# Optimization experiments

Hardware: AMD Instinct MI355X
Metric: run time of the kernel (lower is better)

## Reference

```python
import jax, jax.numpy as jnp
import numpy as np

B, N, L, D = 64, 512, 12, 128   # batch, nodes, neighbors, node_dim==edge_dim
Z = 3 * D                        # 2*node_dim + edge_dim
NC = 3                           # n_convs
VOCAB = 1000
BN_EPS = 1e-3                    # keras BatchNormalization default epsilon


def setup_inputs() -> dict:
    key = jax.random.key(0)
    ks = jax.random.split(key, 14)
    inp = {}
    inp['node_types'] = jax.random.randint(ks[0], (B, N), 0, VOCAB)
    inp['neighbor_list'] = jax.random.randint(ks[1], (B, N, L), 0, N)
    inp['edge_types'] = jax.random.randint(ks[2], (B, N, L), 0, VOCAB)
    inp['slot_types'] = jax.random.normal(ks[3], (B, N, D), jnp.float32)
    inp['node_w'] = jax.random.normal(ks[4], (VOCAB, D), jnp.float32) * 0.1
    inp['edge_w'] = jax.random.normal(ks[5], (VOCAB, D), jnp.float32) * 0.1
    inp['wf'] = jax.random.normal(ks[6], (NC, Z, D), jnp.float32) * 0.05
    inp['bf'] = jax.random.normal(ks[7], (NC, D), jnp.float32) * 0.01
    inp['ws'] = jax.random.normal(ks[8], (NC, Z, D), jnp.float32) * 0.05
    inp['bs'] = jax.random.normal(ks[9], (NC, D), jnp.float32) * 0.01
    inp['bn_gamma'] = jnp.ones((NC, D), jnp.float32)
    inp['bn_beta'] = jnp.zeros((NC, D), jnp.float32)
    inp['bn_mean'] = jax.random.normal(ks[10], (NC, D), jnp.float32) * 0.01
    inp['bn_var'] = jax.random.uniform(ks[11], (NC, D), jnp.float32, 0.5, 1.5)
    inp['dense_w'] = jax.random.normal(ks[12], (D, 1), jnp.float32) * 0.1
    inp['dense_b'] = jnp.zeros((1,), jnp.float32)
    return inp


def _embed(w, x):
    # gather with negative-index masking, as in Embedding.call (inference path)
    idx = jnp.where(x < 0, 0, x)
    mask = (x >= 0).astype(jnp.float32)[..., None]
    return w[idx] * mask


def reference(node_types, neighbor_list, edge_types, slot_types,
              node_w, edge_w, wf, bf, ws, bs,
              bn_gamma, bn_beta, bn_mean, bn_var, dense_w, dense_b):
    v = _embed(node_w, node_types) + slot_types          # (B, N, D)
    e = _embed(edge_w, edge_types)                       # (B, N, L, D)

    nl = neighbor_list
    n_safe = jnp.where(nl < 0, 0, nl)                    # (B, N, L)
    nmask = (nl >= 0).astype(jnp.float32)[..., None]     # (B, N, L, 1)

    for i in range(NC):
        # neighbor gather: per-batch index into node axis
        nn = jax.vmap(lambda vv, ii: vv[ii])(v, n_safe) * nmask  # (B, N, L, D)
        v_view = jnp.broadcast_to(v[:, :, None, :], nn.shape)
        z = jnp.concatenate([v_view, nn, e], axis=-1)            # (B, N, L, Z)
        s = (jax.nn.sigmoid(jnp.einsum('bnlz,zd->bnld', z, wf[i]) + bf[i])
             * jnp.tanh(jnp.einsum('bnlz,zd->bnld', z, ws[i]) + bs[i])
             * nmask)
        v_next = v + jnp.sum(s, axis=2)                          # (B, N, D)

        # masked batchnorm (inference: moving stats); invalid rows -> 0
        vf = v_next.reshape(-1, D)
        valid = jnp.all(jnp.abs(vf) > 1e-5, axis=-1)
        bn = bn_gamma[i] * (vf - bn_mean[i]) * jax.lax.rsqrt(bn_var[i] + BN_EPS) + bn_beta[i]
        v = jnp.where(valid[:, None], bn, 0.0).reshape(B, N, D)

    # masked mean pooling over nodes
    pmask = (node_types >= 0).astype(jnp.float32)[..., None]     # (B, N, 1)
    pooled = jnp.sum(v * pmask, axis=1) / jnp.sum(pmask, axis=1)  # (B, D)
    return pooled @ dense_w + dense_b                            # (B, 1)
```

## Files before the change

### kernel.cpp

```cpp
#include <hip/hip_runtime.h>

#define NB 64
#define NN 512
#define NL 12
#define ND 128
#define NZ 384
#define NCONV 3
#define VOCAB 1000
#define BN_EPS 1e-3f
#define LO_SCALE 2048.0f
#define INV_LO (1.0f/2048.0f)
#define SCF (-1.4426950408889634f)
#define SCS ( 2.8853900817779268f)

typedef _Float16 f16;
using half8 = __attribute__((ext_vector_type(8))) _Float16;
using floatx16 = __attribute__((ext_vector_type(16))) float;

__device__ __forceinline__ floatx16 mfma32(half8 a, half8 b, floatx16 c) {
    return __builtin_amdgcn_mfma_f32_32x32x16_f16(a, b, c, 0, 0, 0);
}
__device__ __forceinline__ void split1(float x, f16& h, f16& l) {
    h = (f16)x; l = (f16)((x - (float)h) * LO_SCALE);
}

__global__ __launch_bounds__(256) void setup_kernel(
    const float* __restrict__ wf, const float* __restrict__ wsg,
    f16* __restrict__ Wc_hi, f16* __restrict__ Wc_lo,
    const float* __restrict__ edge_w, float* __restrict__ EWp,
    const int* __restrict__ node_types, const float* __restrict__ slot_types,
    const float* __restrict__ node_w, f16* __restrict__ vhi, f16* __restrict__ vlo)
{
    __shared__ float se[32][128];
    const int blk = blockIdx.x;
    const int tid = threadIdx.x;
    if (blk < 768) {
        int id = blk * 256 + tid;
        int c = id >> 16;
        int rem = id & 65535;
        int col = rem >> 7, k = rem & 127;
        int part = col >> 7;
        int d = col & 127;
        int z = (part < 2) ? (128 + k) : k;
        const float* W = (part & 1) ? wsg : wf;
        float wv = W[((size_t)c * NZ + z) * ND + d];
        f16 h, l; split1(wv, h, l);
        size_t dst = (size_t)c * 65536 + (size_t)(k >> 3) * 4096 + col * 8 + (k & 7);
        Wc_hi[dst] = h; Wc_lo[dst] = l;
    } else if (blk < 864) {
        const int bid = blk - 768;
        const int c = bid >> 5;
        const int tyg = (bid & 31) * 32;
        for (int i = tid; i < 4096; i += 256) {
            int ty = i >> 7, k = i & 127;
            int tyv = tyg + ty;
            se[ty][k] = (tyv < VOCAB) ? edge_w[(size_t)tyv * ND + k] : 0.f;
        }
        __syncthreads();
        const int h = tid >> 7, col = tid & 127;
        const float* W = h ? wsg : wf;
        const float sc = h ? SCS : SCF;
        float acc[32];
        #pragma unroll
        for (int ty = 0; ty < 32; ++ty) acc[ty] = 0.f;
        #pragma unroll 4
        for (int k = 0; k < 128; ++k) {
            float wv = W[((size_t)c * NZ + 256 + k) * ND + col];
            #pragma unroll
            for (int ty = 0; ty < 32; ++ty) acc[ty] = fmaf(se[ty][k], wv, acc[ty]);
        }
        #pragma unroll
        for (int ty = 0; ty < 32; ++ty) {
            int tyv = tyg + ty;
            if (tyv <= VOCAB)
                EWp[((size_t)c * (VOCAB + 1) + tyv) * 256 + (col & 63) * 4 + (col >> 6) * 2 + h] = acc[ty] * sc;
        }
    } else {
        int i = (blk - 864) * 256 + tid;
        int bn = i >> 7, d = i & 127;
        int ty = node_types[bn];
        float m = ty >= 0 ? 1.f : 0.f;
        int idx = ty >= 0 ? ty : 0;
        float v = node_w[(size_t)idx * ND + d] * m + slot_types[i];
        f16 h, l; split1(v, h, l);
        vhi[i] = h; vlo[i] = l;
    }
}

__global__ __launch_bounds__(256, 3) void psgemm_kernel(
    const f16* __restrict__ vhi, const f16* __restrict__ vlo,
    const f16* __restrict__ Wc_hi, const f16* __restrict__ Wc_lo,
    const float* __restrict__ bfv, const float* __restrict__ bsv,
    float* __restrict__ Ppk, float* __restrict__ Spk)
{
    __shared__ __align__(16) char sA[16384];
    const int hw = blockIdx.x;
    const int xcd = hw & 7;
    const int q = hw >> 3;
    const int bl = q >> 5;
    const int r = q & 31;
    const int half = r >> 4;
    const int xloc = r & 15;
    const int batch = bl * 8 + xcd;
    const int node0 = batch * NN + xloc * 32;

    const int tid = threadIdx.x;
    const int lane = tid & 63, w = tid >> 6;
    const int l31 = lane & 31, l32 = lane >> 5;

    #pragma unroll
    for (int it = 0; it < 2; ++it) {
        int slot = it * 256 + tid;
        int rr = slot >> 4, cc = slot & 15;
        int cs = cc ^ (rr & 15);
        size_t src = (size_t)(node0 + rr) * ND + cs * 8;
        *(half8*)(sA + rr * 256 + cc * 16) = *(const half8*)(vhi + src);
        *(half8*)(sA + 8192 + rr * 256 + cc * 16) = *(const half8*)(vlo + src);
    }
    __syncthreads();

    const int dcol = w * 32 + l31;
    const int col0 = half * 256 + dcol;
    const int col1 = col0 + 128;

    floatx16 a00 = {}, a10 = {}, a01 = {}, a11 = {};

    int ch0 = l32;
    half8 b0h = *(const half8*)(Wc_hi + (size_t)ch0 * 4096 + col0 * 8);
    half8 b0l = *(const half8*)(Wc_lo + (size_t)ch0 * 4096 + col0 * 8);
    half8 b1h = *(const half8*)(Wc_hi + (size_t)ch0 * 4096 + col1 * 8);
    half8 b1l = *(const half8*)(Wc_lo + (size_t)ch0 * 4096 + col1 * 8);

    #pragma unroll
    for (int ks = 0; ks < 8; ++ks) {
        half8 n0h, n0l, n1h, n1l;
        if (ks < 7) {
            int nch = (ks + 1) * 2 + l32;
            n0h = *(const half8*)(Wc_hi + (size_t)nch * 4096 + col0 * 8);
            n0l = *(const half8*)(Wc_lo + (size_t)nch * 4096 + col0 * 8);
            n1h = *(const half8*)(Wc_hi + (size_t)nch * 4096 + col1 * 8);
            n1l = *(const half8*)(Wc_lo + (size_t)nch * 4096 + col1 * 8);
        }
        int qq = (((ks * 2 + l32) ^ (l31 & 15)) << 4);
        half8 ah = *(const half8*)(sA + l31 * 256 + qq);
        half8 al = *(const half8*)(sA + 8192 + l31 * 256 + qq);
        a00 = mfma32(ah, b0h, a00);
        a10 = mfma32(ah, b0l, a10);
        a10 = mfma32(al, b0h, a10);
        a01 = mfma32(ah, b1h, a01);
        a11 = mfma32(ah, b1l, a11);
        a11 = mfma32(al, b1h, a11);
        b0h = n0h; b0l = n0l; b1h = n1h; b1l = n1l;
    }

    float bx = 0.f, by = 0.f;
    if (half) { bx = bfv[dcol]; by = bsv[dcol]; }
    float* outp = half ? Spk : Ppk;
    const int dsub = (dcol & 63) * 4 + (dcol >> 6) * 2;
    #pragma unroll
    for (int rr = 0; rr < 16; ++rr) {
        int orow = (rr & 3) + 8 * (rr >> 2) + 4 * l32;
        float2 v2 = { (a00[rr] + a10[rr] * INV_LO + bx) * SCF,
                      (a01[rr] + a11[rr] * INV_LO + by) * SCS };
        *(float2*)(outp + (size_t)(node0 + orow) * 256 + dsub) = v2;
    }
}

__global__ __launch_bounds__(256, 4) void edge_epilogue_kernel(
    f16* __restrict__ vhi, f16* __restrict__ vlo,
    const int* __restrict__ neighbor_list, const int* __restrict__ edge_types,
    const float* __restrict__ Ppk, const float* __restrict__ Spk,
    const float* __restrict__ EWp,
    const float* __restrict__ bn_gamma, const float* __restrict__ bn_beta,
    const float* __restrict__ bn_mean, const float* __restrict__ bn_var)
{
    __shared__ float s_red[2][64][2];
    const int hw = blockIdx.x;
    const int xcd = hw & 7;
    const int q = hw >> 3;
    const int b = (q >> 8) * 8 + xcd;
    const int j = q & 255;
    const int node0 = b * NN + j * 2;

    const int tid = threadIdx.x;
    const int w = tid >> 6, ds = tid & 63;
    const int nl_ = w >> 1;
    const int sub = w & 1;
    const int node = node0 + nl_;
    const int bbase = b * NN;

    int nlv = -1, etv = -1;
    if (ds < 6) {
        nlv = neighbor_list[node * NL + sub * 6 + ds];
        etv = edge_types[node * NL + sub * 6 + ds];
    }
    unsigned long long bm = __ballot(nlv >= 0);

    float4 sp4 = *(const float4*)(Spk + (size_t)node * 256 + ds * 4);
    float4 p4[6], e4[6];
    #pragma unroll
    for (int l = 0; l < 6; ++l) {
        int nl_l = __builtin_amdgcn_readlane(nlv, l);
        int et_l = __builtin_amdgcn_readlane(etv, l);
        int ns = (nl_l >= 0) ? (bbase + nl_l) : node;
        int es = (et_l >= 0) ? et_l : VOCAB;
        p4[l] = *(const float4*)(Ppk + (size_t)ns * 256 + ds * 4);
        e4[l] = *(const float4*)(EWp + (size_t)es * 256 + ds * 4);
    }

    float sum0 = 0.f, sum1 = 0.f;
    #pragma unroll
    for (int l = 0; l < 6; ++l) {
        float m = ((bm >> l) & 1) ? 1.f : 0.f;
        float ax = p4[l].x + sp4.x + e4[l].x;
        float ay = p4[l].y + sp4.y + e4[l].y;
        float az = p4[l].z + sp4.z + e4[l].z;
        float aw = p4[l].w + sp4.w + e4[l].w;
        float u0 = __builtin_amdgcn_exp2f(fminf(ax, 60.f));
        float w0 = __builtin_amdgcn_exp2f(fminf(ay, 60.f));
        float u1 = __builtin_amdgcn_exp2f(fminf(az, 60.f));
        float w1 = __builtin_amdgcn_exp2f(fminf(aw, 60.f));
        float r0 = __builtin_amdgcn_rcpf(fmaf(u0, w0, 1.f + u0 + w0));
        float r1 = __builtin_amdgcn_rcpf(fmaf(u1, w1, 1.f + u1 + w1));
        sum0 = fmaf((w0 - 1.f) * r0, m, sum0);
        sum1 = fmaf((w1 - 1.f) * r1, m, sum1);
    }

    if (sub) { s_red[nl_][ds][0] = sum0; s_red[nl_][ds][1] = sum1; }
    __syncthreads();
    if (!sub) {
        sum0 += s_red[nl_][ds][0];
        sum1 += s_red[nl_][ds][1];
        size_t i0 = (size_t)node * ND + ds;
        size_t i1 = i0 + 64;
        float x0 = (float)vhi[i0] + (float)vlo[i0] * INV_LO + sum0;
        float x1 = (float)vhi[i1] + (float)vlo[i1] * INV_LO + sum1;
        int valid = __all(fabsf(x0) > 1e-5f && fabsf(x1) > 1e-5f);

        float gm0 = bn_gamma[ds], be0 = bn_beta[ds], mu0 = bn_mean[ds];
        float gm1 = bn_gamma[ds + 64], be1 = bn_beta[ds + 64], mu1 = bn_mean[ds + 64];
        float rs0 = __builtin_amdgcn_rcpf(sqrtf(bn_var[ds] + BN_EPS));
        float rs1 = __builtin_amdgcn_rcpf(sqrtf(bn_var[ds + 64] + BN_EPS));
        float o0 = valid ? (gm0 * (x0 - mu0) * rs0 + be0) : 0.f;
        float o1 = valid ? (gm1 * (x1 - mu1) * rs1 + be1) : 0.f;
        f16 h, l2;
        split1(o0, h, l2); vhi[i0] = h; vlo[i0] = l2;
        split1(o1, h, l2); vhi[i1] = h; vlo[i1] = l2;
    }
}

__global__ __launch_bounds__(256) void pool1_kernel(
    const f16* __restrict__ vhi, const f16* __restrict__ vlo,
    const int* __restrict__ node_types, float* __restrict__ partial)
{
    __shared__ float sbuf[128];
    const int b = blockIdx.x >> 3, chunk = blockIdx.x & 7;
    const int d = threadIdx.x & 127, sub = threadIdx.x >> 7;
    const int n0 = chunk * 64 + sub * 32;
    float sum = 0.f;
    #pragma unroll 4
    for (int i = 0; i < 32; ++i) {
        int n = n0 + i;
        int ty = node_types[b * NN + n];
        float mk = ty >= 0 ? 1.f : 0.f;
        size_t ix = ((size_t)(b * NN + n)) * ND + d;
        sum += ((float)vhi[ix] + (float)vlo[ix] * INV_LO) * mk;
    }
    if (sub == 0) sbuf[d] = sum;
    __syncthreads();
    if (sub == 1) partial[(size_t)blockIdx.x * 128 + d] = sbuf[d] + sum;
}

__global__ __launch_bounds__(128) void pool2_kernel(
    const float* __restrict__ partial, const int* __restrict__ node_types,
    const float* __restrict__ dense_w, const float* __restrict__ dense_b,
    float* __restrict__ out)
{
    __shared__ float s_part[2], s_cnt[2];
    const int b = blockIdx.x;
    const int d = threadIdx.x;
    float sum = 0.f;
    #pragma unroll
    for (int c = 0; c < 8; ++c) sum += partial[(size_t)(b * 8 + c) * 128 + d];
    float cnt = 0.f;
    #pragma unroll
    for (int i = 0; i < 4; ++i)
        cnt += (node_types[b * NN + d + i * 128] >= 0) ? 1.f : 0.f;
    #pragma unroll
    for (int off = 32; off > 0; off >>= 1) cnt += __shfl_xor(cnt, off);
    if ((d & 63) == 0) s_cnt[d >> 6] = cnt;
    __syncthreads();
    float tcnt = s_cnt[0] + s_cnt[1];
    float pv = (sum / tcnt) * dense_w[d];
    #pragma unroll
    for (int off = 32; off > 0; off >>= 1) pv += __shfl_down(pv, off);
    if ((d & 63) == 0) s_part[d >> 6] = pv;
    __syncthreads();
    if (d == 0) out[b] = s_part[0] + s_part[1] + dense_b[0];
}

extern "C" void kernel_launch(void* const* d_in, const int* in_sizes, int n_in,
                              void* d_out, int out_size, void* d_ws, size_t ws_size,
                              hipStream_t stream) {
    const int*   node_types    = (const int*)d_in[0];
    const int*   neighbor_list = (const int*)d_in[1];
    const int*   edge_types    = (const int*)d_in[2];
    const float* slot_types    = (const float*)d_in[3];
    const float* node_w        = (const float*)d_in[4];
    const float* edge_w        = (const float*)d_in[5];
    const float* wf            = (const float*)d_in[6];
    const float* bfv           = (const float*)d_in[7];
    const float* wsg           = (const float*)d_in[8];
    const float* bsv           = (const float*)d_in[9];
    const float* bn_gamma      = (const float*)d_in[10];
    const float* bn_beta       = (const float*)d_in[11];
    const float* bn_mean       = (const float*)d_in[12];
    const float* bn_var        = (const float*)d_in[13];
    const float* dense_w       = (const float*)d_in[14];
    const float* dense_b       = (const float*)d_in[15];
    float* out = (float*)d_out;

    float* wsf = (float*)d_ws;
    float* Ppk = wsf;
    float* Spk = wsf + 8388608;
    float* EWp = wsf + 2 * 8388608;
    float* pp  = EWp + 768768;
    f16* f16b  = (f16*)(pp + 65536);
    f16* vhiA  = f16b;
    f16* vloA  = vhiA + 4194304;
    f16* Wc_hi = vloA + 4194304;
    f16* Wc_lo = Wc_hi + 196608;

    setup_kernel<<<17248, 256, 0, stream>>>(
        wf, wsg, Wc_hi, Wc_lo, edge_w, EWp,
        node_types, slot_types, node_w, vhiA, vloA);

    for (int c = 0; c < NCONV; ++c) {
        psgemm_kernel<<<2048, 256, 0, stream>>>(
            vhiA, vloA, Wc_hi + (size_t)c * 65536, Wc_lo + (size_t)c * 65536,
            bfv + c * ND, bsv + c * ND, Ppk, Spk);
        edge_epilogue_kernel<<<16384, 256, 0, stream>>>(
            vhiA, vloA, neighbor_list, edge_types,
            Ppk, Spk, EWp + (size_t)c * (VOCAB + 1) * 256,
            bn_gamma + c * ND, bn_beta + c * ND, bn_mean + c * ND, bn_var + c * ND);
    }

    pool1_kernel<<<NB * 8, 256, 0, stream>>>(vhiA, vloA, node_types, pp);
    pool2_kernel<<<NB, 128, 0, stream>>>(pp, node_types, dense_w, dense_b, out);
}
```

Baseline: 247.7 us.

## Store node state as fp32, precompute BN params, deepen B prefetch, merge pooling

Node features are now kept in a single fp32 buffer instead of separate fp16 hi/lo halves. The hi/lo split moves into the GEMM's shared-memory load, and the edge epilogue and pooling read fp32 directly. Batchnorm scale and shift are precomputed once in setup as packed float4 values, replacing the per-call rsqrt work. The weight fragment prefetch becomes a three-stage ring, a sched_barrier is added after the gathers, and the two pooling kernels are merged into one 512-thread kernel. The GEMM A loads double in bytes, the split arithmetic now happens inside the GEMM, and the single pool kernel runs only 64 blocks.

```diff
diff --git a/kernel.cpp b/kernel.cpp
--- a/kernel.cpp
+++ b/kernel.cpp
@@ -28,8 +28,11 @@
     const float* __restrict__ wf, const float* __restrict__ wsg,
     f16* __restrict__ Wc_hi, f16* __restrict__ Wc_lo,
     const float* __restrict__ edge_w, float* __restrict__ EWp,
+    const float* __restrict__ bn_gamma, const float* __restrict__ bn_beta,
+    const float* __restrict__ bn_mean, const float* __restrict__ bn_var,
+    float* __restrict__ bnp,
     const int* __restrict__ node_types, const float* __restrict__ slot_types,
-    const float* __restrict__ node_w, f16* __restrict__ vhi, f16* __restrict__ vlo)
+    const float* __restrict__ node_w, float* __restrict__ vA)
 {
     __shared__ float se[32][128];
     const int blk = blockIdx.x;
@@ -75,20 +78,29 @@
             if (tyv <= VOCAB)
                 EWp[((size_t)c * (VOCAB + 1) + tyv) * 256 + (col & 63) * 4 + (col >> 6) * 2 + h] = acc[ty] * sc;
         }
+    } else if (blk < 866) {
+        int t = (blk - 864) * 256 + tid;
+        if (t < NCONV * ND) {
+            int c = t >> 7, j = t & 127;
+            float4 q;
+            q.x = bn_gamma[c * ND + j];
+            q.y = bn_beta[c * ND + j];
+            q.z = bn_mean[c * ND + j];
+            q.w = 1.f / sqrtf(bn_var[c * ND + j] + BN_EPS);
+            *(float4*)(bnp + (size_t)t * 4) = q;
+        }
     } else {
-        int i = (blk - 864) * 256 + tid;
+        int i = (blk - 866) * 256 + tid;
         int bn = i >> 7, d = i & 127;
         int ty = node_types[bn];
         float m = ty >= 0 ? 1.f : 0.f;
         int idx = ty >= 0 ? ty : 0;
-        float v = node_w[(size_t)idx * ND + d] * m + slot_types[i];
-        f16 h, l; split1(v, h, l);
-        vhi[i] = h; vlo[i] = l;
+        vA[i] = node_w[(size_t)idx * ND + d] * m + slot_types[i];
     }
 }
 
 __global__ __launch_bounds__(256, 3) void psgemm_kernel(
-    const f16* __restrict__ vhi, const f16* __restrict__ vlo,
+    const float* __restrict__ vA,
     const f16* __restrict__ Wc_hi, const f16* __restrict__ Wc_lo,
     const float* __restrict__ bfv, const float* __restrict__ bsv,
     float* __restrict__ Ppk, float* __restrict__ Spk)
@@ -113,9 +125,18 @@
         int slot = it * 256 + tid;
         int rr = slot >> 4, cc = slot & 15;
         int cs = cc ^ (rr & 15);
-        size_t src = (size_t)(node0 + rr) * ND + cs * 8;
-        *(half8*)(sA + rr * 256 + cc * 16) = *(const half8*)(vhi + src);
-        *(half8*)(sA + 8192 + rr * 256 + cc * 16) = *(const half8*)(vlo + src);
+        const float* vp = vA + (size_t)(node0 + rr) * ND + cs * 8;
+        float4 u0 = *(const float4*)vp;
+        float4 u1 = *(const float4*)(vp + 4);
+        float uu[8] = {u0.x, u0.y, u0.z, u0.w, u1.x, u1.y, u1.z, u1.w};
+        half8 hh, ll;
+        #pragma unroll
+        for (int jj = 0; jj < 8; ++jj) {
+            f16 h, l; split1(uu[jj], h, l);
+            hh[jj] = h; ll[jj] = l;
+        }
+        *(half8*)(sA + rr * 256 + cc * 16) = hh;
+        *(half8*)(sA + 8192 + rr * 256 + cc * 16) = ll;
     }
     __syncthreads();
 
@@ -125,33 +146,31 @@
 
     floatx16 a00 = {}, a10 = {}, a01 = {}, a11 = {};
 
-    int ch0 = l32;
-    half8 b0h = *(const half8*)(Wc_hi + (size_t)ch0 * 4096 + col0 * 8);
-    half8 b0l = *(const half8*)(Wc_lo + (size_t)ch0 * 4096 + col0 * 8);
-    half8 b1h = *(const half8*)(Wc_hi + (size_t)ch0 * 4096 + col1 * 8);
-    half8 b1l = *(const half8*)(Wc_lo + (size_t)ch0 * 4096 + col1 * 8);
+    half8 B[3][4];
+    #define LDB(dst, ks) { \
+        size_t k0 = (size_t)((ks) * 2 + l32) * 4096; \
+        (dst)[0] = *(const half8*)(Wc_hi + k0 + col0 * 8); \
+        (dst)[1] = *(const half8*)(Wc_lo + k0 + col0 * 8); \
+        (dst)[2] = *(const half8*)(Wc_hi + k0 + col1 * 8); \
+        (dst)[3] = *(const half8*)(Wc_lo + k0 + col1 * 8); }
+    LDB(B[0], 0)
+    LDB(B[1], 1)
 
     #pragma unroll
     for (int ks = 0; ks < 8; ++ks) {
-        half8 n0h, n0l, n1h, n1l;
-        if (ks < 7) {
-            int nch = (ks + 1) * 2 + l32;
-            n0h = *(const half8*)(Wc_hi + (size_t)nch * 4096 + col0 * 8);
-            n0l = *(const half8*)(Wc_lo + (size_t)nch * 4096 + col0 * 8);
-            n1h = *(const half8*)(Wc_hi + (size_t)nch * 4096 + col1 * 8);
-            n1l = *(const half8*)(Wc_lo + (size_t)nch * 4096 + col1 * 8);
-        }
+        if (ks < 6) LDB(B[(ks + 2) % 3], ks + 2)
+        const half8* Bc = B[ks % 3];
         int qq = (((ks * 2 + l32) ^ (l31 & 15)) << 4);
         half8 ah = *(const half8*)(sA + l31 * 256 + qq);
         half8 al = *(const half8*)(sA + 8192 + l31 * 256 + qq);
-        a00 = mfma32(ah, b0h, a00);
-        a10 = mfma32(ah, b0l, a10);
-        a10 = mfma32(al, b0h, a10);
-        a01 = mfma32(ah, b1h, a01);
-        a11 = mfma32(ah, b1l, a11);
-        a11 = mfma32(al, b1h, a11);
-        b0h = n0h; b0l = n0l; b1h = n1h; b1l = n1l;
-    }
+        a00 = mfma32(ah, Bc[0], a00);
+        a10 = mfma32(ah, Bc[1], a10);
+        a10 = mfma32(al, Bc[0], a10);
+        a01 = mfma32(ah, Bc[2], a01);
+        a11 = mfma32(ah, Bc[3], a11);
+        a11 = mfma32(al, Bc[2], a11);
+    }
+    #undef LDB
 
     float bx = 0.f, by = 0.f;
     if (half) { bx = bfv[dcol]; by = bsv[dcol]; }
@@ -167,12 +186,11 @@
 }
 
 __global__ __launch_bounds__(256, 4) void edge_epilogue_kernel(
-    f16* __restrict__ vhi, f16* __restrict__ vlo,
+    float* __restrict__ vA,
     const int* __restrict__ neighbor_list, const int* __restrict__ edge_types,
     const float* __restrict__ Ppk, const float* __restrict__ Spk,
-    const float* __restrict__ EWp,
-    const float* __restrict__ bn_gamma, const float* __restrict__ bn_beta,
-    const float* __restrict__ bn_mean, const float* __restrict__ bn_var)
+    const float* __restrict__ EWp, const float* __restrict__ bnp,
+    const float* __restrict__ , const float* __restrict__ )
 {
     __shared__ float s_red[2][64][2];
     const int hw = blockIdx.x;
@@ -207,6 +225,7 @@
         p4[l] = *(const float4*)(Ppk + (size_t)ns * 256 + ds * 4);
         e4[l] = *(const float4*)(EWp + (size_t)es * 256 + ds * 4);
     }
+    __builtin_amdgcn_sched_barrier(0);
 
     float sum0 = 0.f, sum1 = 0.f;
     #pragma unroll
@@ -233,70 +252,49 @@
         sum1 += s_red[nl_][ds][1];
         size_t i0 = (size_t)node * ND + ds;
         size_t i1 = i0 + 64;
-        float x0 = (float)vhi[i0] + (float)vlo[i0] * INV_LO + sum0;
-        float x1 = (float)vhi[i1] + (float)vlo[i1] * INV_LO + sum1;
+        float x0 = vA[i0] + sum0;
+        float x1 = vA[i1] + sum1;
         int valid = __all(fabsf(x0) > 1e-5f && fabsf(x1) > 1e-5f);
-
-        float gm0 = bn_gamma[ds], be0 = bn_beta[ds], mu0 = bn_mean[ds];
-        float gm1 = bn_gamma[ds + 64], be1 = bn_beta[ds + 64], mu1 = bn_mean[ds + 64];
-        float rs0 = __builtin_amdgcn_rcpf(sqrtf(bn_var[ds] + BN_EPS));
-        float rs1 = __builtin_amdgcn_rcpf(sqrtf(bn_var[ds + 64] + BN_EPS));
-        float o0 = valid ? (gm0 * (x0 - mu0) * rs0 + be0) : 0.f;
-        float o1 = valid ? (gm1 * (x1 - mu1) * rs1 + be1) : 0.f;
-        f16 h, l2;
-        split1(o0, h, l2); vhi[i0] = h; vlo[i0] = l2;
-        split1(o1, h, l2); vhi[i1] = h; vlo[i1] = l2;
-    }
-}
-
-__global__ __launch_bounds__(256) void pool1_kernel(
-    const f16* __restrict__ vhi, const f16* __restrict__ vlo,
-    const int* __restrict__ node_types, float* __restrict__ partial)
-{
-    __shared__ float sbuf[128];
-    const int b = blockIdx.x >> 3, chunk = blockIdx.x & 7;
-    const int d = threadIdx.x & 127, sub = threadIdx.x >> 7;
-    const int n0 = chunk * 64 + sub * 32;
-    float sum = 0.f;
-    #pragma unroll 4
-    for (int i = 0; i < 32; ++i) {
-        int n = n0 + i;
-        int ty = node_types[b * NN + n];
-        float mk = ty >= 0 ? 1.f : 0.f;
-        size_t ix = ((size_t)(b * NN + n)) * ND + d;
-        sum += ((float)vhi[ix] + (float)vlo[ix] * INV_LO) * mk;
-    }
-    if (sub == 0) sbuf[d] = sum;
-    __syncthreads();
-    if (sub == 1) partial[(size_t)blockIdx.x * 128 + d] = sbuf[d] + sum;
-}
-
-__global__ __launch_bounds__(128) void pool2_kernel(
-    const float* __restrict__ partial, const int* __restrict__ node_types,
+        float4 q0 = *(const float4*)(bnp + (size_t)ds * 4);
+        float4 q1 = *(const float4*)(bnp + (size_t)(ds + 64) * 4);
+        vA[i0] = valid ? (q0.x * (x0 - q0.z) * q0.w + q0.y) : 0.f;
+        vA[i1] = valid ? (q1.x * (x1 - q1.z) * q1.w + q1.y) : 0.f;
+    }
+}
+
+__global__ __launch_bounds__(512) void pool_kernel(
+    const float* __restrict__ vA, const int* __restrict__ node_types,
     const float* __restrict__ dense_w, const float* __restrict__ dense_b,
     float* __restrict__ out)
 {
-    __shared__ float s_part[2], s_cnt[2];
+    __shared__ float s_sum[4][128];
+    __shared__ float s_cnt[4];
+    __shared__ float s_part[2];
     const int b = blockIdx.x;
-    const int d = threadIdx.x;
-    float sum = 0.f;
-    #pragma unroll
-    for (int c = 0; c < 8; ++c) sum += partial[(size_t)(b * 8 + c) * 128 + d];
-    float cnt = 0.f;
-    #pragma unroll
-    for (int i = 0; i < 4; ++i)
-        cnt += (node_types[b * NN + d + i * 128] >= 0) ? 1.f : 0.f;
-    #pragma unroll
-    for (int off = 32; off > 0; off >>= 1) cnt += __shfl_xor(cnt, off);
-    if ((d & 63) == 0) s_cnt[d >> 6] = cnt;
+    const int tid = threadIdx.x;
+    const int d = tid & 127, chunk = tid >> 7;
+    const int nbase = b * NN + chunk * 128;
+    float sum = 0.f, cnt = 0.f;
+    #pragma unroll 4
+    for (int i = 0; i < 128; ++i) {
+        int ty = node_types[nbase + i];
+        float mk = ty >= 0 ? 1.f : 0.f;
+        sum += vA[(size_t)(nbase + i) * ND + d] * mk;
+        cnt += mk;
+    }
+    s_sum[chunk][d] = sum;
+    if (d == 0) s_cnt[chunk] = cnt;
     __syncthreads();
-    float tcnt = s_cnt[0] + s_cnt[1];
-    float pv = (sum / tcnt) * dense_w[d];
-    #pragma unroll
-    for (int off = 32; off > 0; off >>= 1) pv += __shfl_down(pv, off);
-    if ((d & 63) == 0) s_part[d >> 6] = pv;
+    if (chunk == 0) {
+        float tot = s_sum[0][d] + s_sum[1][d] + s_sum[2][d] + s_sum[3][d];
+        float tcnt = s_cnt[0] + s_cnt[1] + s_cnt[2] + s_cnt[3];
+        float pv = (tot / tcnt) * dense_w[d];
+        #pragma unroll
+        for (int off = 32; off > 0; off >>= 1) pv += __shfl_down(pv, off);
+        if ((d & 63) == 0) s_part[d >> 6] = pv;
+    }
     __syncthreads();
-    if (d == 0) out[b] = s_part[0] + s_part[1] + dense_b[0];
+    if (tid == 0) out[b] = s_part[0] + s_part[1] + dense_b[0];
 }
 
 extern "C" void kernel_launch(void* const* d_in, const int* in_sizes, int n_in,
@@ -324,27 +322,25 @@
     float* Ppk = wsf;
     float* Spk = wsf + 8388608;
     float* EWp = wsf + 2 * 8388608;
-    float* pp  = EWp + 768768;
-    f16* f16b  = (f16*)(pp + 65536);
-    f16* vhiA  = f16b;
-    f16* vloA  = vhiA + 4194304;
-    f16* Wc_hi = vloA + 4194304;
+    float* bnp = EWp + 768768;
+    float* vA  = bnp + 1536;
+    f16* Wc_hi = (f16*)(vA + 4194304);
     f16* Wc_lo = Wc_hi + 196608;
 
-    setup_kernel<<<17248, 256, 0, stream>>>(
+    setup_kernel<<<17250, 256, 0, stream>>>(
         wf, wsg, Wc_hi, Wc_lo, edge_w, EWp,
-        node_types, slot_types, node_w, vhiA, vloA);
+        bn_gamma, bn_beta, bn_mean, bn_var, bnp,
+        node_types, slot_types, node_w, vA);
 
     for (int c = 0; c < NCONV; ++c) {
         psgemm_kernel<<<2048, 256, 0, stream>>>(
-            vhiA, vloA, Wc_hi + (size_t)c * 65536, Wc_lo + (size_t)c * 65536,
+            vA, Wc_hi + (size_t)c * 65536, Wc_lo + (size_t)c * 65536,
             bfv + c * ND, bsv + c * ND, Ppk, Spk);
         edge_epilogue_kernel<<<16384, 256, 0, stream>>>(
-            vhiA, vloA, neighbor_list, edge_types,
+            vA, neighbor_list, edge_types,
             Ppk, Spk, EWp + (size_t)c * (VOCAB + 1) * 256,
-            bn_gamma + c * ND, bn_beta + c * ND, bn_mean + c * ND, bn_var + c * ND);
-    }
-
-    pool1_kernel<<<NB * 8, 256, 0, stream>>>(vhiA, vloA, node_types, pp);
-    pool2_kernel<<<NB, 128, 0, stream>>>(pp, node_types, dense_w, dense_b, out);
-}
+            bnp + (size_t)c * 512, nullptr, nullptr);
+    }
+
+    pool_kernel<<<NB, 512, 0, stream>>>(vA, node_types, dense_w, dense_b, out);
+}
```

Measured after the change: 245.7 us. Within noise of the previous version (-0.8%).
